# Performance work log

Hardware: AMD Instinct MI355X
Metric: run time of the kernel (lower is better)

Reference implementation:

```python
import jax, jax.numpy as jnp
import numpy as np

N_EDGE = 1_000_000
N_NODE = 100_000
EDGE_DIM = 64
N_RADIAL = 16
UP_DIM = 256


def silu(x):
    return x * jax.nn.sigmoid(x)  # Swish(beta=1.0)


def setup_inputs() -> dict:
    key = jax.random.key(0)
    ks = jax.random.split(key, 12)
    s = 0.05
    return {
        "x": jax.random.normal(ks[0], (N_EDGE, EDGE_DIM), jnp.float32),
        "rbf": jax.random.normal(ks[1], (N_EDGE, N_RADIAL), jnp.float32),
        "idx_i": jax.random.randint(ks[2], (N_EDGE,), 0, N_NODE, jnp.int32).astype(jnp.int64),
        "num_nodes": N_NODE,
        "W_rbf": jax.random.normal(ks[3], (N_RADIAL, EDGE_DIM), jnp.float32) * s,
        "W_up": jax.random.normal(ks[4], (EDGE_DIM, UP_DIM), jnp.float32) * s,
        "W1": jax.random.normal(ks[5], (UP_DIM, UP_DIM), jnp.float32) * s,
        "b1": jnp.zeros((UP_DIM,), jnp.float32),
        "W2": jax.random.normal(ks[6], (UP_DIM, UP_DIM), jnp.float32) * s,
        "b2": jnp.zeros((UP_DIM,), jnp.float32),
        "W3": jax.random.normal(ks[7], (UP_DIM, UP_DIM), jnp.float32) * s,
        "b3": jnp.zeros((UP_DIM,), jnp.float32),
        "W_out": jax.random.normal(ks[8], (UP_DIM, 1), jnp.float32) * s,
    }


def reference(x, rbf, idx_i, num_nodes, W_rbf, W_up, W1, b1, W2, b2, W3, b3, W_out):
    # Gate edge embeddings by rbf projection, scatter-add to center nodes.
    e = (rbf @ W_rbf) * x                              # (n_edge, edge_dim)
    h = jax.ops.segment_sum(e, idx_i, num_segments=num_nodes)  # (n_node, edge_dim)
    h = h @ W_up                                       # (n_node, up_dim)
    h = silu(h @ W1 + b1)
    h = silu(h @ W2 + b2)
    h = silu(h @ W3 + b3)
    return h @ W_out                                   # (n_node, out_dim)
```

## Files before the change

### kernel.cpp

```cpp
#include <hip/hip_runtime.h>
#include <hip/hip_bf16.h>

#define EDGE_DIM 64
#define UPD 256

typedef __attribute__((ext_vector_type(8))) short bf16x8;
typedef __attribute__((ext_vector_type(4))) float f32x4;

__device__ __forceinline__ short f2bf(float v) {
    __hip_bfloat16 b = __float2bfloat16(v);
    return *(short*)&b;
}
__device__ __forceinline__ float bf2f(short s) {
    __hip_bfloat16 b = *(__hip_bfloat16*)&s;
    return __bfloat162float(b);
}

__device__ __forceinline__ void split_trunc(float v, short& hi, short& lo) {
    unsigned u = __float_as_uint(v);
    unsigned hu = u & 0xFFFF0000u;
    hi = (short)(hu >> 16);
    float rem = v - __uint_as_float(hu);
    lo = (short)(__float_as_uint(rem) >> 16);
}

__device__ __forceinline__ int detect_use64_block(const void* idx_v,
                                                  int n_edge, int nn,
                                                  int* bad_s) {
    if (threadIdx.x == 0) *bad_s = 0;
    __syncthreads();
    const long long* p = (const long long*)idx_v;
    int i = threadIdx.x;
    if (i < 256 && i < n_edge) {
        long long v = p[i];
        if (v < 0 || v >= (long long)nn) *bad_s = 1;
    }
    __syncthreads();
    return !(*bad_s);
}

__global__ __launch_bounds__(256) void count_kernel(
    const void* __restrict__ idx_v, int n_edge, int nn,
    int* __restrict__ count) {
    __shared__ int bad_s;
    const int use64 = detect_use64_block(idx_v, n_edge, nn, &bad_s);
    const long long* i64 = (const long long*)idx_v;
    const int* i32 = (const int*)idx_v;
    for (int e = blockIdx.x * blockDim.x + threadIdx.x; e < n_edge;
         e += gridDim.x * blockDim.x) {
        int n = use64 ? (int)i64[e] : i32[e];
        atomicAdd(&count[n], 1);
    }
}

__global__ __launch_bounds__(256) void scan_a(const int* __restrict__ count,
                                              int* __restrict__ base,
                                              int* __restrict__ partial,
                                              int nn) {
    __shared__ int s[256];
    const int tid = threadIdx.x;
    const int i0 = blockIdx.x * 1024 + tid * 4;
    int c[4], tsum = 0;
#pragma unroll
    for (int j = 0; j < 4; ++j) {
        c[j] = (i0 + j < nn) ? count[i0 + j] : 0;
        tsum += c[j];
    }
    s[tid] = tsum;
    __syncthreads();
    for (int off = 1; off < 256; off <<= 1) {
        int v = (tid >= off) ? s[tid - off] : 0;
        __syncthreads();
        s[tid] += v;
        __syncthreads();
    }
    int run = s[tid] - tsum;
    if (tid == 255) partial[blockIdx.x] = s[255];
#pragma unroll
    for (int j = 0; j < 4; ++j) {
        if (i0 + j < nn) base[i0 + j] = run;
        run += c[j];
    }
}

__global__ __launch_bounds__(256) void scan_b(int* __restrict__ partial,
                                              int nblk) {
    __shared__ int s[256];
    const int tid = threadIdx.x;
    int v = (tid < nblk) ? partial[tid] : 0;
    s[tid] = v;
    __syncthreads();
    for (int off = 1; off < 256; off <<= 1) {
        int u = (tid >= off) ? s[tid - off] : 0;
        __syncthreads();
        s[tid] += u;
        __syncthreads();
    }
    if (tid < nblk) partial[tid] = s[tid] - v;
}

__global__ __launch_bounds__(256) void scan_c(int* __restrict__ base,
                                              int* __restrict__ cursor,
                                              const int* __restrict__ partial,
                                              int nn, int n_edge) {
    const int tid = threadIdx.x;
    const int b = blockIdx.x;
    const int add = partial[b];
    const int i0 = b * 1024 + tid * 4;
#pragma unroll
    for (int j = 0; j < 4; ++j) {
        int i = i0 + j;
        if (i < nn) {
            int v = base[i] + add;
            base[i] = v;
            cursor[i] = v;
        }
    }
    if (b == 0 && tid == 0) base[nn] = n_edge;
}

__global__ __launch_bounds__(256) void fill_order_kernel(
    const void* __restrict__ idx_v, int n_edge, int nn,
    int* __restrict__ cursor, int* __restrict__ order) {
    __shared__ int bad_s;
    const int use64 = detect_use64_block(idx_v, n_edge, nn, &bad_s);
    const long long* i64 = (const long long*)idx_v;
    const int* i32 = (const int*)idx_v;
    for (int e = blockIdx.x * blockDim.x + threadIdx.x; e < n_edge;
         e += gridDim.x * blockDim.x) {
        int n = use64 ? (int)i64[e] : i32[e];
        int p = atomicAdd(&cursor[n], 1);
        order[p] = e;
    }
}

__global__ __launch_bounds__(256) void gather_kernel(
    const float* __restrict__ x, const float* __restrict__ rbf,
    const int* __restrict__ order, const int* __restrict__ base,
    const float* __restrict__ Wrbf, float* __restrict__ h, int nn) {
    const int lane = threadIdx.x & 63;
    float wreg[16];
#pragma unroll
    for (int q = 0; q < 16; ++q) wreg[q] = Wrbf[q * EDGE_DIM + lane];

    const int wid = __builtin_amdgcn_readfirstlane(threadIdx.x >> 6);
    const int gw = blockIdx.x * 4 + wid;
    const int nwaves = gridDim.x * 4;

    for (int n = gw; n < nn; n += nwaves) {
        const int b0 = base[n], b1 = base[n + 1];
        float acc = 0.f;
        int i = b0;
        for (; i + 4 <= b1; i += 4) {
            const int e0 = order[i + 0];
            const int e1 = order[i + 1];
            const int e2 = order[i + 2];
            const int e3 = order[i + 3];
            const float xv0 = x[(size_t)e0 * EDGE_DIM + lane];
            const float xv1 = x[(size_t)e1 * EDGE_DIM + lane];
            const float xv2 = x[(size_t)e2 * EDGE_DIM + lane];
            const float xv3 = x[(size_t)e3 * EDGE_DIM + lane];
            const float* r0 = rbf + (size_t)e0 * 16;
            const float* r1 = rbf + (size_t)e1 * 16;
            const float* r2 = rbf + (size_t)e2 * 16;
            const float* r3 = rbf + (size_t)e3 * 16;
            float s0 = 0.f, s1 = 0.f, s2 = 0.f, s3 = 0.f;
#pragma unroll
            for (int q = 0; q < 16; ++q) {
                s0 = fmaf(r0[q], wreg[q], s0);
                s1 = fmaf(r1[q], wreg[q], s1);
                s2 = fmaf(r2[q], wreg[q], s2);
                s3 = fmaf(r3[q], wreg[q], s3);
            }
            acc = fmaf(s0, xv0, acc);
            acc = fmaf(s1, xv1, acc);
            acc = fmaf(s2, xv2, acc);
            acc = fmaf(s3, xv3, acc);
        }
        for (; i < b1; ++i) {
            const int e = order[i];
            const float xv = x[(size_t)e * EDGE_DIM + lane];
            const float* rp = rbf + (size_t)e * 16;
            float s = 0.f;
#pragma unroll
            for (int q = 0; q < 16; ++q) s = fmaf(rp[q], wreg[q], s);
            acc = fmaf(s, xv, acc);
        }
        h[(size_t)n * EDGE_DIM + lane] = acc;
    }
}

__device__ __forceinline__ void pack_body(const float* __restrict__ W,
                                          short* __restrict__ out, int t) {
    int l = t & 63, f = t >> 6;
    int kt = f >> 4, nt = f & 15;
    int kbase = kt * 32 + (l >> 4) * 8;
    int col = nt * 16 + (l & 15);
#pragma unroll
    for (int j = 0; j < 8; ++j) {
        float v = W[(kbase + j) * UPD + col];
        short hb = f2bf(v);
        short lb = f2bf(v - bf2f(hb));
        out[f * 1024 + l * 8 + j] = hb;
        out[f * 1024 + 512 + l * 8 + j] = lb;
    }
}

__global__ __launch_bounds__(256) void pack_all_kernel(
    const float* __restrict__ Wup, const float* __restrict__ W1,
    const float* __restrict__ W2, const float* __restrict__ W3,
    short* __restrict__ oup, short* __restrict__ o1, short* __restrict__ o2,
    short* __restrict__ o3) {
    const int b = blockIdx.x;
    if (b < 8) {
        pack_body(Wup, oup, b * 256 + threadIdx.x);
    } else if (b < 40) {
        pack_body(W1, o1, (b - 8) * 256 + threadIdx.x);
    } else if (b < 72) {
        pack_body(W2, o2, (b - 40) * 256 + threadIdx.x);
    } else {
        pack_body(W3, o3, (b - 72) * 256 + threadIdx.x);
    }
}

template <int NK>
__device__ __forceinline__ void mm_layer(const short* AH, const short* AL,
                                         const short* __restrict__ Wpk,
                                         int lr, int lh, int lane, int wq,
                                         f32x4 acc[4][4]) {
    bf16x8 bc[4][2];
#pragma unroll
    for (int nf = 0; nf < 4; ++nf) {
        const short* p = Wpk + (wq * 4 + nf) * 1024 + lane * 8;
        bc[nf][0] = *(const bf16x8*)(p);
        bc[nf][1] = *(const bf16x8*)(p + 512);
    }
#pragma unroll
    for (int kt = 0; kt < NK; ++kt) {
        bf16x8 a[4][2];
#pragma unroll
        for (int m = 0; m < 4; ++m) {
            int r = m * 16 + lr;
            int ch = (kt * 4 + lh) ^ (r & 7);
            int off = r * 256 + ch * 8;
            a[m][0] = *(const bf16x8*)(AH + off);
            a[m][1] = *(const bf16x8*)(AL + off);
        }
        bf16x8 bn[4][2];
        if (kt + 1 < NK) {
#pragma unroll
            for (int nf = 0; nf < 4; ++nf) {
                const short* p =
                    Wpk + ((kt + 1) * 16 + wq * 4 + nf) * 1024 + lane * 8;
                bn[nf][0] = *(const bf16x8*)(p);
                bn[nf][1] = *(const bf16x8*)(p + 512);
            }
        }
#pragma unroll
        for (int m = 0; m < 4; ++m)
#pragma unroll
            for (int nf = 0; nf < 4; ++nf)
                acc[m][nf] = __builtin_amdgcn_mfma_f32_16x16x32_bf16(
                    a[m][0], bc[nf][0], acc[m][nf], 0, 0, 0);
#pragma unroll
        for (int m = 0; m < 4; ++m)
#pragma unroll
            for (int nf = 0; nf < 4; ++nf)
                acc[m][nf] = __builtin_amdgcn_mfma_f32_16x16x32_bf16(
                    a[m][0], bc[nf][1], acc[m][nf], 0, 0, 0);
#pragma unroll
        for (int m = 0; m < 4; ++m)
#pragma unroll
            for (int nf = 0; nf < 4; ++nf)
                acc[m][nf] = __builtin_amdgcn_mfma_f32_16x16x32_bf16(
                    a[m][1], bc[nf][0], acc[m][nf], 0, 0, 0);
        if (kt + 1 < NK) {
#pragma unroll
            for (int nf = 0; nf < 4; ++nf) {
                bc[nf][0] = bn[nf][0];
                bc[nf][1] = bn[nf][1];
            }
        }
    }
}

template <bool ACT>
__device__ __forceinline__ void epilogue_store(f32x4 acc[4][4], short* AH,
                                               short* AL,
                                               const float* __restrict__ bias,
                                               int lr, int lh, int wq) {
    float bv[4] = {0.f, 0.f, 0.f, 0.f};
    if (bias) {
#pragma unroll
        for (int nf = 0; nf < 4; ++nf) bv[nf] = bias[wq * 64 + nf * 16 + lr];
    }
#pragma unroll
    for (int m = 0; m < 4; ++m)
#pragma unroll
        for (int nf = 0; nf < 4; ++nf) {
            int c = wq * 64 + nf * 16 + lr;
#pragma unroll
            for (int reg = 0; reg < 4; ++reg) {
                float v = acc[m][nf][reg] + bv[nf];
                if (ACT) {
                    float e = __expf(-v);
                    v = v * __builtin_amdgcn_rcpf(1.f + e);
                }
                int r = m * 16 + lh * 4 + reg;
                short hb, lb;
                split_trunc(v, hb, lb);
                int off = r * 256 + (((c >> 3) ^ (r & 7)) * 8) + (c & 7);
                AH[off] = hb;
                AL[off] = lb;
            }
        }
}

__global__ __launch_bounds__(256, 2) void node_mlp_mfma(
    const float* __restrict__ h,
    const short* __restrict__ Wup_pk, const short* __restrict__ W1_pk,
    const short* __restrict__ W2_pk, const short* __restrict__ W3_pk,
    const float* __restrict__ b1, const float* __restrict__ b2,
    const float* __restrict__ b3, const float* __restrict__ W_out,
    float* __restrict__ out, int nn) {
    __shared__ short AH[64 * 256];
    __shared__ short AL[64 * 256];
    __shared__ float Bpart[64 * 4];

    const int tid = threadIdx.x;
    const int lane = tid & 63, wq = tid >> 6;
    const int lr = lane & 15, lh = lane >> 4;
    const int node0 = blockIdx.x * 64;

#pragma unroll
    for (int i = 0; i < 4; ++i) {
        int idx4 = tid + i * 256;
        int r = idx4 >> 4, c4 = idx4 & 15;
        float4 v = {0.f, 0.f, 0.f, 0.f};
        if (node0 + r < nn)
            v = *(const float4*)(h + (size_t)(node0 + r) * EDGE_DIM + c4 * 4);
        short h0, h1, h2, h3, l0, l1, l2, l3;
        split_trunc(v.x, h0, l0);
        split_trunc(v.y, h1, l1);
        split_trunc(v.z, h2, l2);
        split_trunc(v.w, h3, l3);
        int off = r * 256 + (((c4 >> 1) ^ (r & 7)) * 8) + (c4 & 1) * 4;
        uint2 hw, lw;
        hw.x = (unsigned short)h0 | ((unsigned)(unsigned short)h1 << 16);
        hw.y = (unsigned short)h2 | ((unsigned)(unsigned short)h3 << 16);
        lw.x = (unsigned short)l0 | ((unsigned)(unsigned short)l1 << 16);
        lw.y = (unsigned short)l2 | ((unsigned)(unsigned short)l3 << 16);
        *(uint2*)(AH + off) = hw;
        *(uint2*)(AL + off) = lw;
    }
    __syncthreads();

    f32x4 acc[4][4];

#pragma unroll
    for (int m = 0; m < 4; ++m)
#pragma unroll
        for (int n = 0; n < 4; ++n) acc[m][n] = (f32x4){0.f, 0.f, 0.f, 0.f};
    mm_layer<2>(AH, AL, Wup_pk, lr, lh, lane, wq, acc);
    __syncthreads();
    epilogue_store<false>(acc, AH, AL, nullptr, lr, lh, wq);
    __syncthreads();

#pragma unroll
    for (int m = 0; m < 4; ++m)
#pragma unroll
        for (int n = 0; n < 4; ++n) acc[m][n] = (f32x4){0.f, 0.f, 0.f, 0.f};
    mm_layer<8>(AH, AL, W1_pk, lr, lh, lane, wq, acc);
    __syncthreads();
    epilogue_store<true>(acc, AH, AL, b1, lr, lh, wq);
    __syncthreads();

#pragma unroll
    for (int m = 0; m < 4; ++m)
#pragma unroll
        for (int n = 0; n < 4; ++n) acc[m][n] = (f32x4){0.f, 0.f, 0.f, 0.f};
    mm_layer<8>(AH, AL, W2_pk, lr, lh, lane, wq, acc);
    __syncthreads();
    epilogue_store<true>(acc, AH, AL, b2, lr, lh, wq);
    __syncthreads();

#pragma unroll
    for (int m = 0; m < 4; ++m)
#pragma unroll
        for (int n = 0; n < 4; ++n) acc[m][n] = (f32x4){0.f, 0.f, 0.f, 0.f};
    mm_layer<8>(AH, AL, W3_pk, lr, lh, lane, wq, acc);

    float b3v[4], wo[4];
#pragma unroll
    for (int nf = 0; nf < 4; ++nf) {
        int c = wq * 64 + nf * 16 + lr;
        b3v[nf] = b3[c];
        wo[nf] = W_out[c];
    }
#pragma unroll
    for (int m = 0; m < 4; ++m) {
#pragma unroll
        for (int reg = 0; reg < 4; ++reg) {
            float s = 0.f;
#pragma unroll
            for (int nf = 0; nf < 4; ++nf) {
                float v = acc[m][nf][reg] + b3v[nf];
                float e = __expf(-v);
                v = v * __builtin_amdgcn_rcpf(1.f + e);
                s = fmaf(v, wo[nf], s);
            }
            s += __shfl_xor(s, 1);
            s += __shfl_xor(s, 2);
            s += __shfl_xor(s, 4);
            s += __shfl_xor(s, 8);
            if (lr == 0) Bpart[(m * 16 + lh * 4 + reg) * 4 + wq] = s;
        }
    }
    __syncthreads();
    if (tid < 64) {
        float s = Bpart[tid * 4] + Bpart[tid * 4 + 1] + Bpart[tid * 4 + 2] +
                  Bpart[tid * 4 + 3];
        if (node0 + tid < nn) out[node0 + tid] = s;
    }
}

extern "C" void kernel_launch(void* const* d_in, const int* in_sizes, int n_in,
                              void* d_out, int out_size, void* d_ws, size_t ws_size,
                              hipStream_t stream) {
    const float* x     = (const float*)d_in[0];
    const float* rbf   = (const float*)d_in[1];
    const void*  idx   = d_in[2];
    const float* W_rbf = (const float*)d_in[4];
    const float* W_up  = (const float*)d_in[5];
    const float* W1    = (const float*)d_in[6];
    const float* b1    = (const float*)d_in[7];
    const float* W2    = (const float*)d_in[8];
    const float* b2    = (const float*)d_in[9];
    const float* W3    = (const float*)d_in[10];
    const float* b3    = (const float*)d_in[11];
    const float* W_out = (const float*)d_in[12];
    float* out = (float*)d_out;

    const int n_edge = in_sizes[0] / EDGE_DIM;
    const int nn = out_size;

    char* p = (char*)d_ws;
    float* h = (float*)p;            p += (size_t)nn * EDGE_DIM * sizeof(float);
    short* wup_pk = (short*)p;       p += 32 * 1024 * sizeof(short);
    short* w1_pk = (short*)p;        p += 128 * 1024 * sizeof(short);
    short* w2_pk = (short*)p;        p += 128 * 1024 * sizeof(short);
    short* w3_pk = (short*)p;        p += 128 * 1024 * sizeof(short);
    int* count = (int*)p;            p += (size_t)nn * sizeof(int);
    int* base = (int*)p;             p += (size_t)(nn + 1) * sizeof(int);
    int* cursor = (int*)p;           p += (size_t)nn * sizeof(int);
    int* partial = (int*)p;          p += 1024;
    int* order = (int*)p;

    const int nblk_scan = (nn + 1023) / 1024;

    hipMemsetAsync(count, 0, (size_t)nn * sizeof(int), stream);
    pack_all_kernel<<<104, 256, 0, stream>>>(W_up, W1, W2, W3, wup_pk, w1_pk,
                                             w2_pk, w3_pk);
    count_kernel<<<2048, 256, 0, stream>>>(idx, n_edge, nn, count);
    scan_a<<<nblk_scan, 256, 0, stream>>>(count, base, partial, nn);
    scan_b<<<1, 256, 0, stream>>>(partial, nblk_scan);
    scan_c<<<nblk_scan, 256, 0, stream>>>(base, cursor, partial, nn, n_edge);
    fill_order_kernel<<<2048, 256, 0, stream>>>(idx, n_edge, nn, cursor,
                                                order);
    gather_kernel<<<4096, 256, 0, stream>>>(x, rbf, order, base, W_rbf, h, nn);

    const int nb = (nn + 63) / 64;
    node_mlp_mfma<<<nb, 256, 0, stream>>>(h, wup_pk, w1_pk, w2_pk, w3_pk,
                                          b1, b2, b3, W_out, out, nn);
}
```

Baseline: 369.7 us.

## Replace per-node gather with edge-chunked segmented sum using atomic flushes

The per-node gather loop is replaced by a kernel in which each wave takes 64 consecutive sorted edge slots. It loads 16 x rows at a time to get more memory-level parallelism and computes the rbf gate by broadcasting one coalesced rbf load through readlane. Partial sums are flushed to h with atomicAdd whenever the node changes, which balances work across waves regardless of node degree. This adds a memset of h, a nodeof array written in fill_order, and float atomics whose ordering makes results nondeterministic.

After: 356.1 us. -3.7%, faster.

```diff
diff --git a/kernel.cpp b/kernel.cpp
--- a/kernel.cpp
+++ b/kernel.cpp
@@ -121,7 +121,8 @@
 
 __global__ __launch_bounds__(256) void fill_order_kernel(
     const void* __restrict__ idx_v, int n_edge, int nn,
-    int* __restrict__ cursor, int* __restrict__ order) {
+    int* __restrict__ cursor, int* __restrict__ order,
+    int* __restrict__ nodeof) {
     __shared__ int bad_s;
     const int use64 = detect_use64_block(idx_v, n_edge, nn, &bad_s);
     const long long* i64 = (const long long*)idx_v;
@@ -131,62 +132,65 @@
         int n = use64 ? (int)i64[e] : i32[e];
         int p = atomicAdd(&cursor[n], 1);
         order[p] = e;
-    }
-}
-
-__global__ __launch_bounds__(256) void gather_kernel(
+        nodeof[p] = n;
+    }
+}
+
+__global__ __launch_bounds__(256) void segsum2_kernel(
     const float* __restrict__ x, const float* __restrict__ rbf,
-    const int* __restrict__ order, const int* __restrict__ base,
-    const float* __restrict__ Wrbf, float* __restrict__ h, int nn) {
+    const int* __restrict__ order, const int* __restrict__ nodeof,
+    const float* __restrict__ Wrbf, float* __restrict__ h, int n_edge) {
     const int lane = threadIdx.x & 63;
     float wreg[16];
 #pragma unroll
     for (int q = 0; q < 16; ++q) wreg[q] = Wrbf[q * EDGE_DIM + lane];
 
-    const int wid = __builtin_amdgcn_readfirstlane(threadIdx.x >> 6);
-    const int gw = blockIdx.x * 4 + wid;
-    const int nwaves = gridDim.x * 4;
-
-    for (int n = gw; n < nn; n += nwaves) {
-        const int b0 = base[n], b1 = base[n + 1];
+    const int wid = threadIdx.x >> 6;
+    const int nchunks = (n_edge + 63) >> 6;
+    const int stride = gridDim.x * 4;
+
+    for (int c = blockIdx.x * 4 + wid; c < nchunks; c += stride) {
+        const int s0 = c * 64;
+        int slot = s0 + lane;
+        if (slot >= n_edge) slot = n_edge - 1;
+        const int ev = order[slot];
+        const int ndv = nodeof[slot];
+
         float acc = 0.f;
-        int i = b0;
-        for (; i + 4 <= b1; i += 4) {
-            const int e0 = order[i + 0];
-            const int e1 = order[i + 1];
-            const int e2 = order[i + 2];
-            const int e3 = order[i + 3];
-            const float xv0 = x[(size_t)e0 * EDGE_DIM + lane];
-            const float xv1 = x[(size_t)e1 * EDGE_DIM + lane];
-            const float xv2 = x[(size_t)e2 * EDGE_DIM + lane];
-            const float xv3 = x[(size_t)e3 * EDGE_DIM + lane];
-            const float* r0 = rbf + (size_t)e0 * 16;
-            const float* r1 = rbf + (size_t)e1 * 16;
-            const float* r2 = rbf + (size_t)e2 * 16;
-            const float* r3 = rbf + (size_t)e3 * 16;
-            float s0 = 0.f, s1 = 0.f, s2 = 0.f, s3 = 0.f;
-#pragma unroll
-            for (int q = 0; q < 16; ++q) {
-                s0 = fmaf(r0[q], wreg[q], s0);
-                s1 = fmaf(r1[q], wreg[q], s1);
-                s2 = fmaf(r2[q], wreg[q], s2);
-                s3 = fmaf(r3[q], wreg[q], s3);
-            }
-            acc = fmaf(s0, xv0, acc);
-            acc = fmaf(s1, xv1, acc);
-            acc = fmaf(s2, xv2, acc);
-            acc = fmaf(s3, xv3, acc);
-        }
-        for (; i < b1; ++i) {
-            const int e = order[i];
-            const float xv = x[(size_t)e * EDGE_DIM + lane];
-            const float* rp = rbf + (size_t)e * 16;
-            float s = 0.f;
-#pragma unroll
-            for (int q = 0; q < 16; ++q) s = fmaf(rp[q], wreg[q], s);
-            acc = fmaf(s, xv, acc);
-        }
-        h[(size_t)n * EDGE_DIM + lane] = acc;
+        int cur = -1;
+#pragma unroll
+        for (int g = 0; g < 4; ++g) {
+            const int j0 = g * 16;
+            int e[16];
+            float xv[16], rv[16];
+#pragma unroll
+            for (int j = 0; j < 16; ++j) {
+                e[j] = __builtin_amdgcn_readlane(ev, j0 + j);
+                xv[j] = x[(size_t)e[j] * EDGE_DIM + lane];
+                rv[j] = rbf[(size_t)e[j] * 16 + (lane & 15)];
+            }
+#pragma unroll
+            for (int j = 0; j < 16; ++j) {
+                float gate = 0.f;
+#pragma unroll
+                for (int q = 0; q < 16; ++q) {
+                    int rb = __builtin_amdgcn_readlane(
+                        __float_as_int(rv[j]), q);
+                    gate = fmaf(__int_as_float(rb), wreg[q], gate);
+                }
+                const int nd = __builtin_amdgcn_readlane(ndv, j0 + j);
+                if (s0 + j0 + j < n_edge) {
+                    if (nd != cur) {
+                        if (cur >= 0)
+                            atomicAdd(&h[(size_t)cur * EDGE_DIM + lane], acc);
+                        cur = nd;
+                        acc = 0.f;
+                    }
+                    acc = fmaf(gate, xv[j], acc);
+                }
+            }
+        }
+        if (cur >= 0) atomicAdd(&h[(size_t)cur * EDGE_DIM + lane], acc);
     }
 }
 
@@ -454,10 +458,12 @@
     int* base = (int*)p;             p += (size_t)(nn + 1) * sizeof(int);
     int* cursor = (int*)p;           p += (size_t)nn * sizeof(int);
     int* partial = (int*)p;          p += 1024;
-    int* order = (int*)p;
+    int* order = (int*)p;            p += (size_t)n_edge * sizeof(int);
+    int* nodeof = (int*)p;
 
     const int nblk_scan = (nn + 1023) / 1024;
 
+    hipMemsetAsync(h, 0, (size_t)nn * EDGE_DIM * sizeof(float), stream);
     hipMemsetAsync(count, 0, (size_t)nn * sizeof(int), stream);
     pack_all_kernel<<<104, 256, 0, stream>>>(W_up, W1, W2, W3, wup_pk, w1_pk,
                                              w2_pk, w3_pk);
@@ -466,8 +472,11 @@
     scan_b<<<1, 256, 0, stream>>>(partial, nblk_scan);
     scan_c<<<nblk_scan, 256, 0, stream>>>(base, cursor, partial, nn, n_edge);
     fill_order_kernel<<<2048, 256, 0, stream>>>(idx, n_edge, nn, cursor,
-                                                order);
-    gather_kernel<<<4096, 256, 0, stream>>>(x, rbf, order, base, W_rbf, h, nn);
+                                                order, nodeof);
+    const int nchunks = (n_edge + 63) / 64;
+    const int nblk_seg = (nchunks + 3) / 4;
+    segsum2_kernel<<<nblk_seg, 256, 0, stream>>>(x, rbf, order, nodeof,
+                                                 W_rbf, h, n_edge);
 
     const int nb = (nn + 63) / 64;
     node_mlp_mfma<<<nb, 256, 0, stream>>>(h, wup_pk, w1_pk, w2_pk, w3_pk,
```
